# Kernel tuning notes

Hardware: AMD Instinct MI355X
Metric: run time of the kernel (lower is better)

Reference implementation:

```python
import jax, jax.numpy as jnp
import numpy as np
from jax import lax

NUM_GRID = 16
THRESHOLD = 0.65
NUM_BG = 1
NUM_FG = 40
MAX_PTS = 42
T, C, H, W = 8, 4, 1024, 1024


def setup_inputs() -> dict:
    key = jax.random.key(0)
    k1, _ = jax.random.split(key)
    similarities = jax.random.uniform(k1, (T, C, H, W), dtype=jnp.float32)
    category_ids = jnp.arange(C, dtype=jnp.int32)
    original_sizes = jnp.full((T, 2), 2048, dtype=jnp.int32)
    return {"similarities": similarities, "category_ids": category_ids,
            "original_sizes": original_sizes}


def _process_one(sim, ori):
    """sim: [H, W] similarity map; ori: [2] original (H, W). Returns ([MAX_PTS,4], count)."""
    h, w = sim.shape
    dt = sim.dtype
    n = h * w
    flat = sim.reshape(-1)
    rows = jnp.arange(n, dtype=jnp.int32) // w   # y coords
    cols = jnp.arange(n, dtype=jnp.int32) % w    # x coords
    neg_inf = jnp.array(-jnp.inf, dtype=dt)

    # ---- foreground: threshold + per-grid-cell best (segment max) ----
    fg_mask = flat > THRESHOLD
    any_fg = jnp.any(fg_mask)
    # replicate original's naming: map_w, map_h = similarity_map.shape
    cell_w = h / NUM_GRID
    cell_h = w / NUM_GRID
    cxi = jnp.clip(jnp.floor(cols / cell_w).astype(jnp.int32), 0, NUM_GRID - 1)
    cyi = jnp.clip(jnp.floor(rows / cell_h).astype(jnp.int32), 0, NUM_GRID - 1)
    cid = cyi * NUM_GRID + cxi                        # [n] grid-cell id
    n_cells = NUM_GRID * NUM_GRID
    mscore = jnp.where(fg_mask, flat, neg_inf)
    cell_max = jax.ops.segment_max(mscore, cid, num_segments=n_cells)   # [n_cells]
    # first (lowest flat index) point achieving the cell max -> torch.topk tie-break
    is_best = fg_mask & (mscore == cell_max[cid])
    cand = jnp.where(is_best, jnp.arange(n, dtype=jnp.int32), n)
    cell_arg = jax.ops.segment_min(cand, cid, num_segments=n_cells)
    cell_valid = jnp.isfinite(cell_max)
    safe = jnp.where(cell_valid, cell_arg, 0)
    px = cols[safe].astype(dt)
    py = rows[safe].astype(dt)
    ps = flat[safe]
    # sort cells by score descending, keep top NUM_FG (filter_foreground_points)
    order = jnp.argsort(-jnp.where(cell_valid, ps, neg_inf))
    top = order[:NUM_FG]
    fg_x, fg_y, fg_s, fg_v = px[top], py[top], ps[top], cell_valid[top]
    n_valid = jnp.minimum(jnp.sum(cell_valid.astype(jnp.int32)), NUM_FG)
    # fallback when nothing exceeds threshold: global argmax (original uses // map_h == // W)
    gidx = jnp.argmax(flat)
    g_y = (gidx // w).astype(dt)
    g_x = (gidx % w).astype(dt)
    g_s = flat[gidx]
    slot0 = jnp.arange(NUM_FG) == 0
    fg_x = jnp.where(any_fg, fg_x, jnp.where(slot0, g_x, 0.0))
    fg_y = jnp.where(any_fg, fg_y, jnp.where(slot0, g_y, 0.0))
    fg_s = jnp.where(any_fg, fg_s, jnp.where(slot0, g_s, 0.0))
    fg_v = jnp.where(any_fg, fg_v, slot0)
    fg_count = jnp.where(any_fg, n_valid, 1)

    # ---- background: k smallest values over the map ----
    neg_vals, bidx = lax.top_k(-flat, NUM_BG)
    b_y = (bidx // w).astype(dt)
    b_x = (bidx % w).astype(dt)
    b_s = -neg_vals

    # ---- convert to original image coordinates ----
    sx = ori[1].astype(dt) / w
    sy = ori[0].astype(dt) / h
    fg_pts = jnp.stack([fg_x * sx, fg_y * sy, fg_s,
                        jnp.ones(NUM_FG, dtype=dt)], axis=-1)
    fg_pts = fg_pts * fg_v[:, None].astype(dt)        # zero out invalid rows
    bg_pts = jnp.stack([b_x * sx, b_y * sy, b_s,
                        jnp.zeros(NUM_BG, dtype=dt)], axis=-1)

    out = jnp.zeros((MAX_PTS, 4), dtype=dt)
    out = out.at[:NUM_FG].set(fg_pts)
    bg_rows = fg_count + jnp.arange(NUM_BG, dtype=jnp.int32)  # bg right after valid fg
    out = out.at[bg_rows].set(bg_pts)
    num = fg_count + NUM_BG
    return out, num


def _forward(similarities, original_sizes):
    per_cat = jax.vmap(_process_one, in_axes=(0, None))      # over C
    per_tgt = jax.vmap(per_cat, in_axes=(0, 0))              # over T
    points, nums = per_tgt(similarities, original_sizes)
    return points, nums.astype(jnp.int32)


def reference(similarities, category_ids, original_sizes):
    # category_ids is metadata (defines C); not used in the point math.
    return _forward(similarities, original_sizes)
```

## Files before the change

kernel.cpp:

```cpp
#include <hip/hip_runtime.h>
#include <math.h>

#define NUM_GRID 16
#define NCELLS   256
#define THRESH   0.65f
#define NUM_FG   40
#define NUM_BG   1
#define MAX_PTS  42
#define T_DIM    8
#define C_DIM    4
#define H_DIM    1024
#define W_DIM    1024
#define NMAPS    (T_DIM * C_DIM)
#define MAP_ELEMS (H_DIM * W_DIM)
#define CELL_DIM 64

__device__ inline void block_reduce_pair(float& v, int& i, bool is_max,
                                         float* sv, int* si, int tid) {
    sv[tid] = v; si[tid] = i;
    __syncthreads();
    for (int s = 128; s > 0; s >>= 1) {
        if (tid < s) {
            float v2 = sv[tid + s]; int i2 = si[tid + s];
            float v1 = sv[tid];     int i1 = si[tid];
            bool take = is_max ? (v2 > v1 || (v2 == v1 && i2 < i1))
                               : (v2 < v1 || (v2 == v1 && i2 < i1));
            if (take) { sv[tid] = v2; si[tid] = i2; }
        }
        __syncthreads();
    }
    v = sv[0]; i = si[0];
    __syncthreads();
}

__global__ __launch_bounds__(256)
void cell_stats_kernel(const float* __restrict__ sim,
                       float* __restrict__ fgmax_o, int* __restrict__ fgarg_o,
                       float* __restrict__ amax_o,  int* __restrict__ amaxarg_o,
                       float* __restrict__ amin_o,  int* __restrict__ aminarg_o) {
    const int b    = blockIdx.x;
    const int map  = b >> 8;
    const int cell = b & 255;
    const int cy   = cell >> 4;
    const int cx   = cell & 15;
    const int tid  = threadIdx.x;
    const int g    = tid & 15;
    const int rr   = tid >> 4;

    const float* base = sim + (size_t)map * MAP_ELEMS;

    float fgv = -INFINITY; int fgi = 0x7fffffff;
    float mxv = -INFINITY; int mxi = 0x7fffffff;
    float mnv =  INFINITY; int mni = 0x7fffffff;

    #pragma unroll
    for (int r = 0; r < 4; ++r) {
        const int row = cy * CELL_DIM + r * 16 + rr;
        const int col = cx * CELL_DIM + g * 4;
        const int idx = row * W_DIM + col;
        const float4 v4 = *reinterpret_cast<const float4*>(base + idx);
        const float vals[4] = {v4.x, v4.y, v4.z, v4.w};
        #pragma unroll
        for (int j = 0; j < 4; ++j) {
            const float v  = vals[j];
            const int   ix = idx + j;
            if (v > mxv) { mxv = v; mxi = ix; }
            if (v < mnv) { mnv = v; mni = ix; }
            if (v > THRESH && v > fgv) { fgv = v; fgi = ix; }
        }
    }

    __shared__ float sv[256];
    __shared__ int   si[256];

    block_reduce_pair(fgv, fgi, true,  sv, si, tid);
    block_reduce_pair(mxv, mxi, true,  sv, si, tid);
    block_reduce_pair(mnv, mni, false, sv, si, tid);

    if (tid == 0) {
        const int o = map * NCELLS + cell;
        fgmax_o[o]   = fgv;  fgarg_o[o]   = fgi;
        amax_o[o]    = mxv;  amaxarg_o[o] = mxi;
        amin_o[o]    = mnv;  aminarg_o[o] = mni;
    }
}

__global__ __launch_bounds__(256)
void select_kernel(const float* __restrict__ fgmax_i, const int* __restrict__ fgarg_i,
                   const float* __restrict__ amax_i,  const int* __restrict__ amaxarg_i,
                   const float* __restrict__ amin_i,  const int* __restrict__ aminarg_i,
                   const int* __restrict__ orig_sizes,
                   float* __restrict__ out_pts, float* __restrict__ out_nums) {
    const int m   = blockIdx.x;
    const int tid = threadIdx.x;
    const int t   = m >> 2;

    const float sx = (float)orig_sizes[t * 2 + 1] / (float)W_DIM;
    const float sy = (float)orig_sizes[t * 2 + 0] / (float)H_DIM;

    const int o = m * NCELLS + tid;
    const float fgv = fgmax_i[o];
    const int   fgi = fgarg_i[o];
    const bool  valid = (fgv > -INFINITY);

    __shared__ float skey[256];
    skey[tid] = fgv;

    __shared__ float sv[256];
    __shared__ int   si[256];

    float gv = amax_i[o]; int gi = amaxarg_i[o];
    block_reduce_pair(gv, gi, true, sv, si, tid);
    float bv = amin_i[o]; int bi = aminarg_i[o];
    block_reduce_pair(bv, bi, false, sv, si, tid);

    const int nvalid = __syncthreads_count(valid ? 1 : 0);
    const bool any_fg = (nvalid > 0);
    const int fg_count = any_fg ? (nvalid < NUM_FG ? nvalid : NUM_FG) : 1;

    int rank = 0;
    const float key = fgv;
    for (int j = 0; j < 256; ++j) {
        const float kj = skey[j];
        rank += (kj > key || (kj == key && j < tid)) ? 1 : 0;
    }

    __shared__ float outp[MAX_PTS * 4];
    if (tid < MAX_PTS * 4) outp[tid] = 0.0f;
    __syncthreads();

    if (any_fg && valid && rank < NUM_FG) {
        const int col = fgi & (W_DIM - 1);
        const int row = fgi >> 10;
        outp[rank * 4 + 0] = (float)col * sx;
        outp[rank * 4 + 1] = (float)row * sy;
        outp[rank * 4 + 2] = fgv;
        outp[rank * 4 + 3] = 1.0f;
    }
    if (!any_fg && tid == 0) {
        const int col = gi & (W_DIM - 1);
        const int row = gi >> 10;
        outp[0] = (float)col * sx;
        outp[1] = (float)row * sy;
        outp[2] = gv;
        outp[3] = 1.0f;
    }
    __syncthreads();

    if (tid == 0) {
        const int col = bi & (W_DIM - 1);
        const int row = bi >> 10;
        outp[fg_count * 4 + 0] = (float)col * sx;
        outp[fg_count * 4 + 1] = (float)row * sy;
        outp[fg_count * 4 + 2] = bv;
        outp[fg_count * 4 + 3] = 0.0f;
    }
    __syncthreads();

    if (tid < MAX_PTS * 4) out_pts[(size_t)m * (MAX_PTS * 4) + tid] = outp[tid];
    if (tid == 0) out_nums[m] = (float)(fg_count + NUM_BG);
}

extern "C" void kernel_launch(void* const* d_in, const int* in_sizes, int n_in,
                              void* d_out, int out_size, void* d_ws, size_t ws_size,
                              hipStream_t stream) {
    const float* sim        = (const float*)d_in[0];
    const int*   orig_sizes = (const int*)d_in[2];

    float* out = (float*)d_out;
    float* out_pts  = out;
    float* out_nums = out + (size_t)NMAPS * MAX_PTS * 4;

    const size_t NC = (size_t)NMAPS * NCELLS;
    char* ws = (char*)d_ws;
    float* fgmax_ws   = (float*)(ws + 0 * NC * 4);
    int*   fgarg_ws   = (int*)  (ws + 1 * NC * 4);
    float* amax_ws    = (float*)(ws + 2 * NC * 4);
    int*   amaxarg_ws = (int*)  (ws + 3 * NC * 4);
    float* amin_ws    = (float*)(ws + 4 * NC * 4);
    int*   aminarg_ws = (int*)  (ws + 5 * NC * 4);

    cell_stats_kernel<<<NMAPS * NCELLS, 256, 0, stream>>>(
        sim, fgmax_ws, fgarg_ws, amax_ws, amaxarg_ws, amin_ws, aminarg_ws);

    select_kernel<<<NMAPS, 256, 0, stream>>>(
        fgmax_ws, fgarg_ws, amax_ws, amaxarg_ws, amin_ws, aminarg_ws,
        orig_sizes, out_pts, out_nums);
}
```

Before: 202.4 us.

## Restructure cell stats into row-strip blocks with wave-shuffle reductions

The first kernel now assigns each block a full-width strip of 16 rows across a grid row, so each thread streams one contiguous float4 column down the strip. Per-cell results come from wave-level xor shuffles instead of shared-memory tree reductions. Four partial results per cell are written to workspace and merged in the select kernel. The separate foreground max is removed, since the cell's foreground max equals its overall max whenever that max exceeds the threshold. The aim is fewer blocks, no shared-memory barriers, and more contiguous loads; the cost is fewer blocks (2048) and more partial results to merge in the select kernel.

```diff
diff --git a/kernel.cpp b/kernel.cpp
--- a/kernel.cpp
+++ b/kernel.cpp
@@ -14,6 +14,59 @@
 #define NMAPS    (T_DIM * C_DIM)
 #define MAP_ELEMS (H_DIM * W_DIM)
 #define CELL_DIM 64
+#define NSPLIT   4
+#define ROWS_PER_SPLIT (CELL_DIM / NSPLIT)
+
+__global__ __launch_bounds__(256)
+void cell_stats_kernel(const float* __restrict__ sim,
+                       float* __restrict__ maxv_o, int* __restrict__ maxi_o,
+                       float* __restrict__ minv_o, int* __restrict__ mini_o) {
+    const int b   = blockIdx.x;
+    const int map = b >> 6;
+    const int cy  = (b >> 2) & 15;
+    const int s   = b & 3;
+    const int tid = threadIdx.x;
+
+    const int row0 = cy * CELL_DIM + s * ROWS_PER_SPLIT;
+    const float* __restrict__ p =
+        sim + (size_t)map * MAP_ELEMS + (size_t)row0 * W_DIM + tid * 4;
+    int ix0 = row0 * W_DIM + tid * 4;
+
+    float mxv = -INFINITY; int mxi = 0x7fffffff;
+    float mnv =  INFINITY; int mni = 0x7fffffff;
+
+    #pragma unroll 4
+    for (int r = 0; r < ROWS_PER_SPLIT; ++r) {
+        const float4 v4 = *reinterpret_cast<const float4*>(p);
+        const float vals[4] = {v4.x, v4.y, v4.z, v4.w};
+        #pragma unroll
+        for (int j = 0; j < 4; ++j) {
+            const float v  = vals[j];
+            const int   ix = ix0 + j;
+            if (v > mxv) { mxv = v; mxi = ix; }
+            if (v < mnv) { mnv = v; mni = ix; }
+        }
+        p   += W_DIM;
+        ix0 += W_DIM;
+    }
+
+    #pragma unroll
+    for (int mask = 1; mask <= 8; mask <<= 1) {
+        float ov = __shfl_xor(mxv, mask, 64);
+        int   oi = __shfl_xor(mxi, mask, 64);
+        if (ov > mxv || (ov == mxv && oi < mxi)) { mxv = ov; mxi = oi; }
+        float uv = __shfl_xor(mnv, mask, 64);
+        int   ui = __shfl_xor(mni, mask, 64);
+        if (uv < mnv || (uv == mnv && ui < mni)) { mnv = uv; mni = ui; }
+    }
+
+    if ((tid & 15) == 0) {
+        const int cx = tid >> 4;
+        const int o  = ((map * NCELLS + cy * NUM_GRID + cx) * NSPLIT) + s;
+        maxv_o[o] = mxv; maxi_o[o] = mxi;
+        minv_o[o] = mnv; mini_o[o] = mni;
+    }
+}
 
 __device__ inline void block_reduce_pair(float& v, int& i, bool is_max,
                                          float* sv, int* si, int tid) {
@@ -34,61 +87,8 @@
 }
 
 __global__ __launch_bounds__(256)
-void cell_stats_kernel(const float* __restrict__ sim,
-                       float* __restrict__ fgmax_o, int* __restrict__ fgarg_o,
-                       float* __restrict__ amax_o,  int* __restrict__ amaxarg_o,
-                       float* __restrict__ amin_o,  int* __restrict__ aminarg_o) {
-    const int b    = blockIdx.x;
-    const int map  = b >> 8;
-    const int cell = b & 255;
-    const int cy   = cell >> 4;
-    const int cx   = cell & 15;
-    const int tid  = threadIdx.x;
-    const int g    = tid & 15;
-    const int rr   = tid >> 4;
-
-    const float* base = sim + (size_t)map * MAP_ELEMS;
-
-    float fgv = -INFINITY; int fgi = 0x7fffffff;
-    float mxv = -INFINITY; int mxi = 0x7fffffff;
-    float mnv =  INFINITY; int mni = 0x7fffffff;
-
-    #pragma unroll
-    for (int r = 0; r < 4; ++r) {
-        const int row = cy * CELL_DIM + r * 16 + rr;
-        const int col = cx * CELL_DIM + g * 4;
-        const int idx = row * W_DIM + col;
-        const float4 v4 = *reinterpret_cast<const float4*>(base + idx);
-        const float vals[4] = {v4.x, v4.y, v4.z, v4.w};
-        #pragma unroll
-        for (int j = 0; j < 4; ++j) {
-            const float v  = vals[j];
-            const int   ix = idx + j;
-            if (v > mxv) { mxv = v; mxi = ix; }
-            if (v < mnv) { mnv = v; mni = ix; }
-            if (v > THRESH && v > fgv) { fgv = v; fgi = ix; }
-        }
-    }
-
-    __shared__ float sv[256];
-    __shared__ int   si[256];
-
-    block_reduce_pair(fgv, fgi, true,  sv, si, tid);
-    block_reduce_pair(mxv, mxi, true,  sv, si, tid);
-    block_reduce_pair(mnv, mni, false, sv, si, tid);
-
-    if (tid == 0) {
-        const int o = map * NCELLS + cell;
-        fgmax_o[o]   = fgv;  fgarg_o[o]   = fgi;
-        amax_o[o]    = mxv;  amaxarg_o[o] = mxi;
-        amin_o[o]    = mnv;  aminarg_o[o] = mni;
-    }
-}
-
-__global__ __launch_bounds__(256)
-void select_kernel(const float* __restrict__ fgmax_i, const int* __restrict__ fgarg_i,
-                   const float* __restrict__ amax_i,  const int* __restrict__ amaxarg_i,
-                   const float* __restrict__ amin_i,  const int* __restrict__ aminarg_i,
+void select_kernel(const float* __restrict__ maxv_i, const int* __restrict__ maxi_i,
+                   const float* __restrict__ minv_i, const int* __restrict__ mini_i,
                    const int* __restrict__ orig_sizes,
                    float* __restrict__ out_pts, float* __restrict__ out_nums) {
     const int m   = blockIdx.x;
@@ -98,10 +98,20 @@
     const float sx = (float)orig_sizes[t * 2 + 1] / (float)W_DIM;
     const float sy = (float)orig_sizes[t * 2 + 0] / (float)H_DIM;
 
-    const int o = m * NCELLS + tid;
-    const float fgv = fgmax_i[o];
-    const int   fgi = fgarg_i[o];
-    const bool  valid = (fgv > -INFINITY);
+    float mxv = -INFINITY; int mxi = 0x7fffffff;
+    float mnv =  INFINITY; int mni = 0x7fffffff;
+    const int base = (m * NCELLS + tid) * NSPLIT;
+    #pragma unroll
+    for (int s = 0; s < NSPLIT; ++s) {
+        const float ov = maxv_i[base + s]; const int oi = maxi_i[base + s];
+        if (ov > mxv || (ov == mxv && oi < mxi)) { mxv = ov; mxi = oi; }
+        const float uv = minv_i[base + s]; const int ui = mini_i[base + s];
+        if (uv < mnv || (uv == mnv && ui < mni)) { mnv = uv; mni = ui; }
+    }
+
+    const bool  valid = (mxv > THRESH);
+    const float fgv   = valid ? mxv : -INFINITY;
+    const int   fgi   = mxi;
 
     __shared__ float skey[256];
     skey[tid] = fgv;
@@ -109,9 +119,9 @@
     __shared__ float sv[256];
     __shared__ int   si[256];
 
-    float gv = amax_i[o]; int gi = amaxarg_i[o];
+    float gv = mxv; int gi = mxi;
     block_reduce_pair(gv, gi, true, sv, si, tid);
-    float bv = amin_i[o]; int bi = aminarg_i[o];
+    float bv = mnv; int bi = mni;
     block_reduce_pair(bv, bi, false, sv, si, tid);
 
     const int nvalid = __syncthreads_count(valid ? 1 : 0);
@@ -171,19 +181,17 @@
     float* out_pts  = out;
     float* out_nums = out + (size_t)NMAPS * MAX_PTS * 4;
 
-    const size_t NC = (size_t)NMAPS * NCELLS;
+    const size_t NP = (size_t)NMAPS * NCELLS * NSPLIT;
     char* ws = (char*)d_ws;
-    float* fgmax_ws   = (float*)(ws + 0 * NC * 4);
-    int*   fgarg_ws   = (int*)  (ws + 1 * NC * 4);
-    float* amax_ws    = (float*)(ws + 2 * NC * 4);
-    int*   amaxarg_ws = (int*)  (ws + 3 * NC * 4);
-    float* amin_ws    = (float*)(ws + 4 * NC * 4);
-    int*   aminarg_ws = (int*)  (ws + 5 * NC * 4);
+    float* maxv_ws = (float*)(ws + 0 * NP * 4);
+    int*   maxi_ws = (int*)  (ws + 1 * NP * 4);
+    float* minv_ws = (float*)(ws + 2 * NP * 4);
+    int*   mini_ws = (int*)  (ws + 3 * NP * 4);
 
-    cell_stats_kernel<<<NMAPS * NCELLS, 256, 0, stream>>>(
-        sim, fgmax_ws, fgarg_ws, amax_ws, amaxarg_ws, amin_ws, aminarg_ws);
+    cell_stats_kernel<<<NMAPS * NUM_GRID * NSPLIT, 256, 0, stream>>>(
+        sim, maxv_ws, maxi_ws, minv_ws, mini_ws);
 
     select_kernel<<<NMAPS, 256, 0, stream>>>(
-        fgmax_ws, fgarg_ws, amax_ws, amaxarg_ws, amin_ws, aminarg_ws,
+        maxv_ws, maxi_ws, minv_ws, mini_ws,
         orig_sizes, out_pts, out_nums);
 }
```

Measured after the change: 203.7 us. About the same (+0.6%).
